# Performance work log

Measured on AMD Instinct MI355X. Metric: run time of the kernel, lower is better.

## Reference

```python
import jax, jax.numpy as jnp
import numpy as np
from jax import lax

VOCAB = 400000
D = 300          # embedding_dim
L = 2000         # seq len
B = 4            # batch
C1, K1 = 64, 3   # conv1 outChan, kernel
C2, K2 = 128, 500
HID = 256
NCLS = 5


def setup_inputs() -> dict:
    key = jax.random.key(0)
    ks = jax.random.split(key, 8)
    x = jax.random.randint(ks[0], (B, L), 0, VOCAB)
    emb_table = jax.random.normal(ks[1], (VOCAB, D), jnp.float32) * 0.1
    conv1_w = jax.random.normal(ks[2], (C1, 1, K1), jnp.float32) * 0.1
    conv1_b = jnp.zeros((C1,), jnp.float32)
    conv2_w = jax.random.normal(ks[3], (C2, C1, K2), jnp.float32) * 0.02
    conv2_b = jnp.zeros((C2,), jnp.float32)
    lin1_w = jax.random.normal(ks[4], (HID, C2), jnp.float32) * 0.05
    lin1_b = jnp.zeros((HID,), jnp.float32)
    lin2_w = jax.random.normal(ks[5], (NCLS, HID), jnp.float32) * 0.05
    lin2_b = jnp.zeros((NCLS,), jnp.float32)
    return dict(x=x, emb_table=emb_table,
                conv1_w=conv1_w, conv1_b=conv1_b,
                conv2_w=conv2_w, conv2_b=conv2_b,
                lin1_w=lin1_w, lin1_b=lin1_b,
                lin2_w=lin2_w, lin2_b=lin2_b)


def _conv1d(x, w):
    # x: [N, Cin, W]; w: [Cout, Cin, K]; VALID, stride 1
    return lax.conv_general_dilated(x, w, window_strides=(1,), padding='VALID',
                                    dimension_numbers=('NCH', 'OIH', 'NCH'))


def _maxpool1d(x, k):
    # kernel == stride (torch MaxPool1d default)
    return lax.reduce_window(x, -jnp.inf, lax.max, (1, 1, k), (1, 1, k), 'VALID')


def reference(x, emb_table, conv1_w, conv1_b, conv2_w, conv2_b,
              lin1_w, lin1_b, lin2_w, lin2_b):
    emb = emb_table[x]                                  # [B, L, D]
    # concat module == reshape to [B, 1, L*D]
    out = emb.reshape(emb.shape[0], 1, emb.shape[1] * emb.shape[2])
    out = _conv1d(out, conv1_w) + conv1_b[None, :, None]  # [B, C1, L*D-K1+1]
    out = _maxpool1d(jax.nn.relu(out), D)                 # pool 300
    out = _conv1d(out, conv2_w) + conv2_b[None, :, None]  # [B, C2, 1500]
    out = _maxpool1d(jax.nn.relu(out), D * 5)             # pool 1500 -> len 1
    out = out.reshape(out.shape[0], -1)                   # [B, C2]
    out = jax.nn.relu(out @ lin1_w.T + lin1_b)            # [B, HID]
    out = jax.nn.softmax(out @ lin2_w.T + lin2_b, axis=-1)  # [B, 5]
    # Dropout is identity in eval mode
    return out
```

## Files before the change

kernel.cpp:

```cpp
#include <hip/hip_runtime.h>
#include <hip/hip_bf16.h>
#include <math.h>

#define VOCAB 400000
#define D     300
#define L     2000
#define B     4
#define C1    64
#define C2    128
#define K2    500
#define HID   256
#define NCLS  5
#define NP1   1999
#define T2    1500
#define TPAD  2304
#define S     8
#define CI    8
#define NK2   125
#define BN    192
#define NTI   8
#define NKT   1600

typedef __attribute__((ext_vector_type(8))) short short8v;
typedef __attribute__((ext_vector_type(4))) float f32x4;

__device__ __forceinline__ void gload_lds16(const void* g, void* l) {
    __builtin_amdgcn_global_load_lds(
        (const __attribute__((address_space(1))) void*)g,
        (__attribute__((address_space(3))) void*)l, 16, 0, 0);
}

__global__ __launch_bounds__(256) void k_prep(
    const int* __restrict__ x, const float* __restrict__ emb,
    const float* __restrict__ w1, const float* __restrict__ b1,
    const float* __restrict__ w2,
    __hip_bfloat16* __restrict__ in1T, __hip_bfloat16* __restrict__ aT)
{
    __shared__ float smem[2560];
    int bid = blockIdx.x, tid = threadIdx.x;
    if (bid < NKT) {
        int s  = bid / 200;
        int rem = bid % 200;
        int kc = rem / 8, cog = rem % 8;
        int co0 = cog * 16;
        for (int i = tid; i < 2560; i += 256) {
            int co_l = i / 160, r = i % 160, ci = r / 20, kl = r % 20;
            smem[i] = w2[((size_t)(co0 + co_l) * C1 + s * CI + ci) * K2 + kc * 20 + kl];
        }
        __syncthreads();
        for (int u = tid; u < 320; u += 256) {
            int co_l = u & 15, gk = u >> 4;
            int g = gk & 3, k2l = gk >> 2;
            __hip_bfloat16 tmp[8];
#pragma unroll
            for (int e = 0; e < 8; ++e)
                tmp[e] = __float2bfloat16(smem[co_l * 160 + e * 20 + 4 * k2l + g]);
            size_t off = ((size_t)((s * NK2 + kc * 5 + k2l) * 4 + g)) * 1024
                       + (size_t)(co0 + co_l) * 8;
            *reinterpret_cast<int4*>(aT + off) = *reinterpret_cast<const int4*>(tmp);
        }
    } else {
        int blk = bid - NKT;
        int b = blk / NP1, p = blk % NP1;
        float* sig = smem;
        float* red = smem + 304;
        int row0 = x[b * L + p];
        int row1 = x[b * L + p + 1];
        if (tid < 76) {
            const float* src = (tid < 75) ? (emb + (size_t)row0 * D + 4 * tid)
                                          : (emb + (size_t)row1 * D);
            *reinterpret_cast<float4*>(sig + 4 * tid) =
                *reinterpret_cast<const float4*>(src);
        }
        __syncthreads();
        int c = tid & 63, g = tid >> 6;
        float wa = w1[c * 3 + 0], wb = w1[c * 3 + 1], wc = w1[c * 3 + 2];
        float bb = b1[c];
        int jb = 76 * g;
        int ns = (g < 3) ? 19 : 18;
        float m = -INFINITY;
        float4 cur = *reinterpret_cast<float4*>(sig + jb);
        for (int st = 0; st < ns; ++st) {
            float4 nxt = *reinterpret_cast<float4*>(sig + jb + 4 * st + 4);
            float xx[8] = {cur.x, cur.y, cur.z, cur.w, nxt.x, nxt.y, nxt.z, nxt.w};
#pragma unroll
            for (int q = 0; q < 4; ++q) {
                float v = fmaf(wc, xx[q + 2], fmaf(wb, xx[q + 1], fmaf(wa, xx[q], bb)));
                m = fmaxf(m, v);
            }
            cur = nxt;
        }
        red[g * 64 + c] = m;
        __syncthreads();
        if (tid < 64) {
            float mm = fmaxf(fmaxf(red[tid], red[64 + tid]),
                             fmaxf(red[128 + tid], red[192 + tid]));
            int sg = tid >> 3, ci = tid & 7;
            in1T[((size_t)(b * S + sg) * TPAD + p) * CI + ci] =
                __float2bfloat16(fmaxf(mm, 0.0f));
        }
    }
}

__global__ __launch_bounds__(256, 1) void k2_mfma(
    const __hip_bfloat16* __restrict__ in1T,
    const __hip_bfloat16* __restrict__ aT,
    float* __restrict__ part)
{
    int bid = blockIdx.x;
    int s = bid & 7;
    int rem = bid >> 3;
    int b = rem >> 3, ti = rem & 7;
    int t0 = ti * BN;

    __shared__ __align__(16) __hip_bfloat16 seg[768 * CI];

    int tid = threadIdx.x;
    int w = tid >> 6, l = tid & 63;
    int lane16 = l & 15, g = l >> 4;
    int co0w = (w & 1) * 64;
    int tn0  = (w >> 1) * 96;

    {
        const char* gsrc = (const char*)(in1T + ((size_t)(b * S + s) * TPAD + t0) * CI);
        char* lb = (char*)seg + w * 1024;
#pragma unroll
        for (int r = 0; r < 3; ++r)
            gload_lds16(gsrc + (size_t)(r * 256 + tid) * 16, lb + r * 4096);
    }
    __syncthreads();

    const __hip_bfloat16* abase =
        aT + (size_t)s * NK2 * 4096 + g * 1024 + (co0w + lane16) * 8;

    f32x4 acc[4][6];
#pragma unroll
    for (int fa = 0; fa < 4; ++fa)
#pragma unroll
        for (int fb = 0; fb < 6; ++fb) acc[fa][fb] = (f32x4){0.f, 0.f, 0.f, 0.f};

#define LOADA(AR, KK)                                                         \
    {                                                                         \
        _Pragma("unroll")                                                     \
        for (int fa = 0; fa < 4; ++fa)                                        \
            AR[fa] = *reinterpret_cast<const short8v*>(                       \
                abase + (size_t)(KK) * 4096 + fa * 128);                      \
    }

#define STEP(AR, KK)                                                          \
    {                                                                         \
        short8v bfr[6];                                                       \
        _Pragma("unroll")                                                     \
        for (int fb = 0; fb < 6; ++fb)                                        \
            bfr[fb] = *reinterpret_cast<const short8v*>(                      \
                seg + (size_t)(tn0 + fb * 16 + lane16 + 4 * (KK) + g) * 8);   \
        _Pragma("unroll")                                                     \
        for (int fa = 0; fa < 4; ++fa) {                                      \
            _Pragma("unroll")                                                 \
            for (int fb = 0; fb < 6; ++fb)                                    \
                acc[fa][fb] = __builtin_amdgcn_mfma_f32_16x16x32_bf16(        \
                    AR[fa], bfr[fb], acc[fa][fb], 0, 0, 0);                   \
        }                                                                     \
    }

    short8v a0[4], a1[4];
    LOADA(a0, 0);
    LOADA(a1, 1);
    int k2 = 0;
#pragma unroll 1
    for (; k2 + 3 < NK2; k2 += 2) {
        STEP(a0, k2);
        LOADA(a0, k2 + 2);
        STEP(a1, k2 + 1);
        LOADA(a1, k2 + 3);
    }
    STEP(a0, k2);
    LOADA(a0, k2 + 2);
    STEP(a1, k2 + 1);
    STEP(a0, k2 + 2);

#undef LOADA
#undef STEP

#pragma unroll
    for (int fa = 0; fa < 4; ++fa) {
#pragma unroll
        for (int fb = 0; fb < 6; ++fb) {
            int t = t0 + tn0 + fb * 16 + lane16;
            if (t < T2) {
                int cob = co0w + fa * 16 + 4 * g;
#pragma unroll
                for (int r = 0; r < 4; ++r)
                    part[((size_t)(s * B + b) * C2 + cob + r) * T2 + t] =
                        acc[fa][fb][r];
            }
        }
    }
}

__global__ __launch_bounds__(256) void k2b_pool(
    const float* __restrict__ part, const float* __restrict__ b2,
    float* __restrict__ h1)
{
    int bc = blockIdx.x;
    int b = bc / C2, co = bc % C2;
    int tid = threadIdx.x;
    float m = -INFINITY;
    for (int t4 = tid; t4 < T2 / 4; t4 += 256) {
        float4 sum = {0.f, 0.f, 0.f, 0.f};
#pragma unroll
        for (int s = 0; s < S; ++s) {
            const float4* p = reinterpret_cast<const float4*>(
                part + ((size_t)(s * B + b) * C2 + co) * T2);
            float4 v = p[t4];
            sum.x += v.x; sum.y += v.y; sum.z += v.z; sum.w += v.w;
        }
        m = fmaxf(m, fmaxf(fmaxf(sum.x, sum.y), fmaxf(sum.z, sum.w)));
    }
    __shared__ float red[256];
    red[tid] = m;
    __syncthreads();
    for (int st = 128; st > 0; st >>= 1) {
        if (tid < st) red[tid] = fmaxf(red[tid], red[tid + st]);
        __syncthreads();
    }
    if (tid == 0) h1[bc] = fmaxf(red[0] + b2[co], 0.0f);
}

__global__ __launch_bounds__(256) void k3_head(
    const float* __restrict__ h1,
    const float* __restrict__ wl1, const float* __restrict__ bl1,
    const float* __restrict__ wl2, const float* __restrict__ bl2,
    float* __restrict__ out)
{
    int b = blockIdx.x;
    int tid = threadIdx.x;
    __shared__ float xin[C2];
    __shared__ float hbuf[HID];
    __shared__ float lg[NCLS];
    if (tid < C2) xin[tid] = h1[b * C2 + tid];
    __syncthreads();
    float a = bl1[tid];
    for (int c = 0; c < C2; ++c) a = fmaf(xin[c], wl1[tid * C2 + c], a);
    hbuf[tid] = fmaxf(a, 0.0f);
    __syncthreads();
    if (tid < NCLS) {
        float lv = bl2[tid];
        for (int j = 0; j < HID; ++j) lv = fmaf(hbuf[j], wl2[tid * HID + j], lv);
        lg[tid] = lv;
    }
    __syncthreads();
    if (tid < NCLS) {
        float mx = lg[0];
        for (int i = 1; i < NCLS; ++i) mx = fmaxf(mx, lg[i]);
        float sum = 0.f;
        for (int i = 0; i < NCLS; ++i) sum += expf(lg[i] - mx);
        out[b * NCLS + tid] = expf(lg[tid] - mx) / sum;
    }
}

extern "C" void kernel_launch(void* const* d_in, const int* in_sizes, int n_in,
                              void* d_out, int out_size, void* d_ws, size_t ws_size,
                              hipStream_t stream)
{
    const int*   x   = (const int*)  d_in[0];
    const float* emb = (const float*)d_in[1];
    const float* w1  = (const float*)d_in[2];
    const float* b1  = (const float*)d_in[3];
    const float* w2  = (const float*)d_in[4];
    const float* b2  = (const float*)d_in[5];
    const float* wl1 = (const float*)d_in[6];
    const float* bl1 = (const float*)d_in[7];
    const float* wl2 = (const float*)d_in[8];
    const float* bl2 = (const float*)d_in[9];
    float* out = (float*)d_out;

    float* ws   = (float*)d_ws;
    float* part = ws;
    float* h1   = ws + (size_t)S * B * C2 * T2;
    __hip_bfloat16* in1T = (__hip_bfloat16*)(h1 + 512);
    __hip_bfloat16* aT   = in1T + (size_t)B * S * TPAD * CI;

    hipLaunchKernelGGL(k_prep, dim3(NKT + B * NP1), dim3(256), 0, stream,
                       x, emb, w1, b1, w2, in1T, aT);
    hipLaunchKernelGGL(k2_mfma, dim3(256), dim3(256), 0, stream, in1T, aT, part);
    hipLaunchKernelGGL(k2b_pool, dim3(B * C2), dim3(256), 0, stream, part, b2, h1);
    hipLaunchKernelGGL(k3_head, dim3(B), dim3(256), 0, stream,
                       h1, wl1, bl1, wl2, bl2, out);
}
```

Before: 92.84 us.

## Batch four pool windows per conv1 block and double k2_mfma waves

The conv1+pool part of k_prep now gives each block four consecutive pool windows instead of one. Each 64-thread group owns a full 300-element window, so the shared-memory cross-group max reduction and its second barrier go away, and about a quarter as many blocks are launched. The k2_mfma kernel moves to 512 threads with each wave computing half as many time columns (3 fragments instead of 6). This raises waves per block for latency hiding, at the cost of fewer MFMAs per A-fragment load, so A-operand traffic per MFMA doubles.

```diff
diff --git a/kernel.cpp b/kernel.cpp
--- a/kernel.cpp
+++ b/kernel.cpp
@@ -18,8 +18,8 @@
 #define CI    8
 #define NK2   125
 #define BN    192
-#define NTI   8
 #define NKT   1600
+#define NC1B  (B * 500)
 
 typedef __attribute__((ext_vector_type(8))) short short8v;
 typedef __attribute__((ext_vector_type(4))) float f32x4;
@@ -61,26 +61,25 @@
         }
     } else {
         int blk = bid - NKT;
-        int b = blk / NP1, p = blk % NP1;
+        int b = blk / 500, pb = blk % 500;
+        int p0 = pb * 4;
         float* sig = smem;
-        float* red = smem + 304;
-        int row0 = x[b * L + p];
-        int row1 = x[b * L + p + 1];
-        if (tid < 76) {
-            const float* src = (tid < 75) ? (emb + (size_t)row0 * D + 4 * tid)
-                                          : (emb + (size_t)row1 * D);
+        if (tid < 301) {
+            int rj = tid / 75, col = (tid % 75) * 4;
+            int xi = p0 + rj; if (xi > L - 1) xi = L - 1;
+            int row = x[b * L + xi];
             *reinterpret_cast<float4*>(sig + 4 * tid) =
-                *reinterpret_cast<const float4*>(src);
+                *reinterpret_cast<const float4*>(emb + (size_t)row * D + col);
         }
         __syncthreads();
-        int c = tid & 63, g = tid >> 6;
+        int c = tid & 63, pg = tid >> 6;
+        int p = p0 + pg;
         float wa = w1[c * 3 + 0], wb = w1[c * 3 + 1], wc = w1[c * 3 + 2];
         float bb = b1[c];
-        int jb = 76 * g;
-        int ns = (g < 3) ? 19 : 18;
+        int jb = 300 * pg;
         float m = -INFINITY;
         float4 cur = *reinterpret_cast<float4*>(sig + jb);
-        for (int st = 0; st < ns; ++st) {
+        for (int st = 0; st < 75; ++st) {
             float4 nxt = *reinterpret_cast<float4*>(sig + jb + 4 * st + 4);
             float xx[8] = {cur.x, cur.y, cur.z, cur.w, nxt.x, nxt.y, nxt.z, nxt.w};
 #pragma unroll
@@ -90,19 +89,15 @@
             }
             cur = nxt;
         }
-        red[g * 64 + c] = m;
-        __syncthreads();
-        if (tid < 64) {
-            float mm = fmaxf(fmaxf(red[tid], red[64 + tid]),
-                             fmaxf(red[128 + tid], red[192 + tid]));
-            int sg = tid >> 3, ci = tid & 7;
+        if (p < NP1) {
+            int sg = c >> 3, ci = c & 7;
             in1T[((size_t)(b * S + sg) * TPAD + p) * CI + ci] =
-                __float2bfloat16(fmaxf(mm, 0.0f));
-        }
-    }
-}
-
-__global__ __launch_bounds__(256, 1) void k2_mfma(
+                __float2bfloat16(fmaxf(m, 0.0f));
+        }
+    }
+}
+
+__global__ __launch_bounds__(512, 1) void k2_mfma(
     const __hip_bfloat16* __restrict__ in1T,
     const __hip_bfloat16* __restrict__ aT,
     float* __restrict__ part)
@@ -119,25 +114,25 @@
     int w = tid >> 6, l = tid & 63;
     int lane16 = l & 15, g = l >> 4;
     int co0w = (w & 1) * 64;
-    int tn0  = (w >> 1) * 96;
+    int tn0  = (w >> 1) * 48;
 
     {
         const char* gsrc = (const char*)(in1T + ((size_t)(b * S + s) * TPAD + t0) * CI);
         char* lb = (char*)seg + w * 1024;
-#pragma unroll
-        for (int r = 0; r < 3; ++r)
-            gload_lds16(gsrc + (size_t)(r * 256 + tid) * 16, lb + r * 4096);
+        gload_lds16(gsrc + (size_t)tid * 16, lb);
+        if (tid < 256)
+            gload_lds16(gsrc + (size_t)(512 + tid) * 16, lb + 8192);
     }
     __syncthreads();
 
     const __hip_bfloat16* abase =
         aT + (size_t)s * NK2 * 4096 + g * 1024 + (co0w + lane16) * 8;
 
-    f32x4 acc[4][6];
+    f32x4 acc[4][3];
 #pragma unroll
     for (int fa = 0; fa < 4; ++fa)
 #pragma unroll
-        for (int fb = 0; fb < 6; ++fb) acc[fa][fb] = (f32x4){0.f, 0.f, 0.f, 0.f};
+        for (int fb = 0; fb < 3; ++fb) acc[fa][fb] = (f32x4){0.f, 0.f, 0.f, 0.f};
 
 #define LOADA(AR, KK)                                                         \
     {                                                                         \
@@ -149,15 +144,15 @@
 
 #define STEP(AR, KK)                                                          \
     {                                                                         \
-        short8v bfr[6];                                                       \
+        short8v bfr[3];                                                       \
         _Pragma("unroll")                                                     \
-        for (int fb = 0; fb < 6; ++fb)                                        \
+        for (int fb = 0; fb < 3; ++fb)                                        \
             bfr[fb] = *reinterpret_cast<const short8v*>(                      \
                 seg + (size_t)(tn0 + fb * 16 + lane16 + 4 * (KK) + g) * 8);   \
         _Pragma("unroll")                                                     \
         for (int fa = 0; fa < 4; ++fa) {                                      \
             _Pragma("unroll")                                                 \
-            for (int fb = 0; fb < 6; ++fb)                                    \
+            for (int fb = 0; fb < 3; ++fb)                                    \
                 acc[fa][fb] = __builtin_amdgcn_mfma_f32_16x16x32_bf16(        \
                     AR[fa], bfr[fb], acc[fa][fb], 0, 0, 0);                   \
         }                                                                     \
@@ -185,7 +180,7 @@
 #pragma unroll
     for (int fa = 0; fa < 4; ++fa) {
 #pragma unroll
-        for (int fb = 0; fb < 6; ++fb) {
+        for (int fb = 0; fb < 3; ++fb) {
             int t = t0 + tn0 + fb * 16 + lane16;
             if (t < T2) {
                 int cob = co0w + fa * 16 + 4 * g;
@@ -281,9 +276,9 @@
     __hip_bfloat16* in1T = (__hip_bfloat16*)(h1 + 512);
     __hip_bfloat16* aT   = in1T + (size_t)B * S * TPAD * CI;
 
-    hipLaunchKernelGGL(k_prep, dim3(NKT + B * NP1), dim3(256), 0, stream,
+    hipLaunchKernelGGL(k_prep, dim3(NKT + NC1B), dim3(256), 0, stream,
                        x, emb, w1, b1, w2, in1T, aT);
-    hipLaunchKernelGGL(k2_mfma, dim3(256), dim3(256), 0, stream, in1T, aT, part);
+    hipLaunchKernelGGL(k2_mfma, dim3(256), dim3(512), 0, stream, in1T, aT, part);
     hipLaunchKernelGGL(k2b_pool, dim3(B * C2), dim3(256), 0, stream, part, b2, h1);
     hipLaunchKernelGGL(k3_head, dim3(B), dim3(256), 0, stream,
                        h1, wl1, bl1, wl2, bl2, out);
```

Result: faster. 82.76 us (-10.9%).
